# Kernel tuning notes

Measured on AMD Instinct MI355X. Metric: run time of the kernel, lower is better.

The kernel has to match this reference:

```python
import jax, jax.numpy as jnp
import numpy as np

N_NODES = 50000
N_EDGES = 800000
D_IN = 256
D_HID = 256
D_OUT = 128


def setup_inputs() -> dict:
    key = jax.random.key(0)
    ks = jax.random.split(key, 6)
    z = jax.random.normal(ks[0], (N_NODES, D_IN), dtype=jnp.float32)
    edge_index = jax.random.randint(ks[1], (2, N_EDGES), 0, N_NODES, dtype=jnp.int32)
    W1 = jax.random.normal(ks[2], (D_IN, D_HID), dtype=jnp.float32) / np.sqrt(D_IN).astype(np.float32)
    b1 = jnp.zeros((D_HID,), dtype=jnp.float32)
    W2 = jax.random.normal(ks[3], (D_HID, D_OUT), dtype=jnp.float32) / np.sqrt(D_HID).astype(np.float32)
    b2 = jnp.zeros((D_OUT,), dtype=jnp.float32)
    return {"z": z, "edge_index": edge_index, "W1": W1, "b1": b1, "W2": W2, "b2": b2}


def _gcn_conv(x, W, b, src, dst, n_nodes):
    """GCNConv: x' = D^{-1/2} (A + I) D^{-1/2} (x W) + b (symmetric norm, self-loops)."""
    x = x @ W  # [n, d_out] dense transform first (as in PyG GCNConv)
    loop = jnp.arange(n_nodes, dtype=src.dtype)
    s = jnp.concatenate([src, loop])  # add self-loops
    d = jnp.concatenate([dst, loop])
    deg = jax.ops.segment_sum(jnp.ones(s.shape, dtype=x.dtype), d, num_segments=n_nodes)
    dinv = jnp.where(deg > 0, jax.lax.rsqrt(deg), 0.0)
    norm = dinv[s] * dinv[d]  # per-edge symmetric normalization
    msgs = x[s] * norm[:, None]  # gather + scale
    out = jax.ops.segment_sum(msgs, d, num_segments=n_nodes)  # scatter-add
    return out + b


def reference(z, edge_index, W1, b1, W2, b2):
    src, dst = edge_index[0], edge_index[1]
    n = z.shape[0]
    h = jax.nn.relu(_gcn_conv(z, W1, b1, src, dst, n))
    return _gcn_conv(h, W2, b2, src, dst, n)
```

## Files before the change

### kernel.cpp

```cpp
#include <hip/hip_runtime.h>


#define N_NODES 50000
#define N_EDGES 800000
#define D_IN    256
#define D_HID   256
#define D_OUT   128

typedef unsigned int uint32;
typedef unsigned short u16;

typedef __attribute__((ext_vector_type(8))) short bf16x8;
typedef __attribute__((ext_vector_type(4))) float f32x4;

__device__ __forceinline__ u16 f2bf_rne(float f) {
    union { float f; uint32 u; } c; c.f = f;
    uint32 u = c.u;
    u += 0x7FFFu + ((u >> 16) & 1u);
    return (u16)(u >> 16);
}
__device__ __forceinline__ float bf_lo(uint32 p) {
    union { uint32 u; float f; } c; c.u = p << 16; return c.f;
}
__device__ __forceinline__ float bf_hi(uint32 p) {
    union { uint32 u; float f; } c; c.u = p & 0xFFFF0000u; return c.f;
}


__global__ __launch_bounds__(256) void prep_kernel(const float* __restrict__ z,
                                                   const int* __restrict__ dst,
                                                   const float* __restrict__ W1,
                                                   const float* __restrict__ W2,
                                                   u16* __restrict__ zb,
                                                   u16* __restrict__ w1t,
                                                   u16* __restrict__ w2t,
                                                   int* __restrict__ cnt) {
    const int g = blockIdx.x * 256 + threadIdx.x;
    const int GT = gridDim.x * 256;

    for (int c = g; c < N_NODES * D_IN / 8; c += GT) {
        int i = c * 8;
        float4 a = *(const float4*)(z + i);
        float4 d = *(const float4*)(z + i + 4);
        uint4 pk;
        pk.x = (uint32)f2bf_rne(a.x) | ((uint32)f2bf_rne(a.y) << 16);
        pk.y = (uint32)f2bf_rne(a.z) | ((uint32)f2bf_rne(a.w) << 16);
        pk.z = (uint32)f2bf_rne(d.x) | ((uint32)f2bf_rne(d.y) << 16);
        pk.w = (uint32)f2bf_rne(d.z) | ((uint32)f2bf_rne(d.w) << 16);
        *(uint4*)(zb + i) = pk;
    }
    for (int idx = g; idx < D_IN * D_HID + D_HID * D_OUT; idx += GT) {
        if (idx < D_IN * D_HID) {
            int nrow = idx >> 8, kcol = idx & 255;
            w1t[idx] = f2bf_rne(W1[kcol * D_HID + nrow]);
        } else {
            int j = idx - D_IN * D_HID;
            int nrow = j >> 8, kcol = j & 255;
            w2t[j] = f2bf_rne(W2[kcol * D_OUT + nrow]);
        }
    }
    for (int i = g; i < N_EDGES; i += GT) atomicAdd(&cnt[dst[i]], 1);
}


__global__ __launch_bounds__(256) void block_sum_kernel(const int* __restrict__ cnt,
                                                        float* __restrict__ dinv,
                                                        int* __restrict__ bsum, int n) {
    int b = blockIdx.x, t = threadIdx.x;
    int i = b * 256 + t;
    int v = 0;
    if (i < n) {
        v = cnt[i];
        dinv[i] = rsqrtf((float)(v + 1));
    }
    int r = v;
    #pragma unroll
    for (int off = 32; off >= 1; off >>= 1) r += __shfl_down(r, off, 64);
    __shared__ int ws[4];
    if ((t & 63) == 0) ws[t >> 6] = r;
    __syncthreads();
    if (t == 0) bsum[b] = ws[0] + ws[1] + ws[2] + ws[3];
}

__global__ __launch_bounds__(256) void scan_partials_kernel(const int* __restrict__ bsum,
                                                            int* __restrict__ boff,
                                                            int* __restrict__ row_ptr,
                                                            int nb, int n) {
    int t = threadIdx.x;
    int v = (t < nb) ? bsum[t] : 0;
    int lane = t & 63, w = t >> 6;
    int x = v;
    #pragma unroll
    for (int off = 1; off < 64; off <<= 1) {
        int u = __shfl_up(x, off, 64);
        if (lane >= off) x += u;
    }
    __shared__ int ws[4];
    if (lane == 63) ws[w] = x;
    __syncthreads();
    int base = 0;
    for (int i = 0; i < w; ++i) base += ws[i];
    int incl = base + x;
    if (t < nb) boff[t] = incl - v;
    if (t == 255) row_ptr[n] = incl;
}

__global__ __launch_bounds__(256) void scan_write_kernel(const int* __restrict__ cnt,
                                                         const int* __restrict__ boff,
                                                         int* __restrict__ row_ptr,
                                                         int* __restrict__ cursor, int n) {
    int b = blockIdx.x, t = threadIdx.x;
    int i = b * 256 + t;
    int v = (i < n) ? cnt[i] : 0;
    int lane = t & 63, w = t >> 6;
    int x = v;
    #pragma unroll
    for (int off = 1; off < 64; off <<= 1) {
        int u = __shfl_up(x, off, 64);
        if (lane >= off) x += u;
    }
    __shared__ int ws[4];
    if (lane == 63) ws[w] = x;
    __syncthreads();
    int base = boff[b];
    for (int i2 = 0; i2 < w; ++i2) base += ws[i2];
    int excl = base + (x - v);
    if (i < n) { row_ptr[i] = excl; cursor[i] = excl; }
}

__global__ void fill_kernel(const int* __restrict__ src, const int* __restrict__ dst,
                            int* __restrict__ cursor, int* __restrict__ col, int n_edges) {
    int i = blockIdx.x * blockDim.x + threadIdx.x;
    if (i < n_edges) {
        int d = dst[i];
        int s = src[i];
        int pos = atomicAdd(&cursor[d], 1);
        col[pos] = s;
    }
}


template <int NT>
__global__ __launch_bounds__(256, 4) void gemm_bf16_kernel(const u16* __restrict__ A,
                                                           const u16* __restrict__ BT,
                                                           u16* __restrict__ C, int M) {
    const int K = 256;
    __shared__ short As[128 * 32];
    __shared__ short Bs[128 * 32];

    const int m0 = blockIdx.x * 128;
    const int n0 = blockIdx.y * 128;
    const int t  = threadIdx.x;
    const int w  = t >> 6;
    const int lane = t & 63;
    const int lm = lane & 15;
    const int lq = lane >> 4;
    const int wm = w & 1;
    const int wn = w >> 1;

    f32x4 acc[4][4] = {};

    for (int k0 = 0; k0 < K; k0 += 32) {
        #pragma unroll
        for (int j = 0; j < 2; ++j) {
            int c = w * 128 + j * 64 + lane;
            int row = c >> 2;
            int kc = k0 + (c & 3) * 8;
            int gm = m0 + row; if (gm >= M) gm = M - 1;
            const u16* gpa = A  + (size_t)gm * K + kc;
            const u16* gpb = BT + (size_t)(n0 + row) * K + kc;
            __builtin_amdgcn_global_load_lds(
                (const __attribute__((address_space(1))) void*)gpa,
                (__attribute__((address_space(3))) void*)(As + (w * 128 + j * 64) * 8),
                16, 0, 0);
            __builtin_amdgcn_global_load_lds(
                (const __attribute__((address_space(1))) void*)gpb,
                (__attribute__((address_space(3))) void*)(Bs + (w * 128 + j * 64) * 8),
                16, 0, 0);
        }
        __syncthreads();

        bf16x8 af[4], bf[4];
        #pragma unroll
        for (int mt = 0; mt < 4; ++mt)
            af[mt] = *(const bf16x8*)&As[(wm * 64 + mt * 16 + lm) * 32 + lq * 8];
        #pragma unroll
        for (int nt = 0; nt < 4; ++nt)
            bf[nt] = *(const bf16x8*)&Bs[(wn * 64 + nt * 16 + lm) * 32 + lq * 8];

        #pragma unroll
        for (int mt = 0; mt < 4; ++mt)
            #pragma unroll
            for (int nt = 0; nt < 4; ++nt)
                acc[mt][nt] = __builtin_amdgcn_mfma_f32_16x16x32_bf16(
                    af[mt], bf[nt], acc[mt][nt], 0, 0, 0);

        __syncthreads();
    }

    #pragma unroll
    for (int mt = 0; mt < 4; ++mt) {
        #pragma unroll
        for (int r = 0; r < 4; ++r) {
            int gm = m0 + wm * 64 + mt * 16 + lq * 4 + r;
            if (gm < M) {
                #pragma unroll
                for (int nt = 0; nt < 4; ++nt) {
                    int gn = n0 + wn * 64 + nt * 16 + lm;
                    C[(size_t)gm * NT + gn] = f2bf_rne(acc[mt][nt][r]);
                }
            }
        }
    }
}


template <int D, int NSPLIT, bool RELU, bool OUTBF>
__global__ __launch_bounds__(256) void aggregate_kernel(const u16* __restrict__ x,
                                                        const int* __restrict__ row_ptr,
                                                        const int* __restrict__ col,
                                                        const float* __restrict__ dinv,
                                                        const float* __restrict__ bias,
                                                        void* __restrict__ outp, int n_nodes) {
    constexpr int DP  = D / NSPLIT;
    constexpr int VPL = DP / 64;
    const int b = blockIdx.x;
    const int part = b % NSPLIT;
    const int node = (b / NSPLIT) * 4 + (threadIdx.x >> 6);
    const int lane = threadIdx.x & 63;
    if (node >= n_nodes) return;
    const int c0 = part * DP + lane * VPL;

    float di = dinv[node];
    float acc[4][VPL] = {};

    {
        float w = di * di;
        const u16* xs = x + (size_t)node * D + c0;
        if constexpr (VPL == 4) {
            uint2 p = *(const uint2*)xs;
            acc[0][0] = bf_lo(p.x) * w;
            acc[0][1] = bf_hi(p.x) * w;
            acc[0][2] = bf_lo(p.y) * w;
            acc[0][3] = bf_hi(p.y) * w;
        } else {
            uint32 p = *(const uint32*)xs;
            acc[0][0] = bf_lo(p) * w;
            acc[0][1] = bf_hi(p) * w;
        }
    }

    int e0 = row_ptr[node], e1 = row_ptr[node + 1];
    int e = e0;
    for (; e + 4 <= e1; e += 4) {
        #pragma unroll
        for (int u = 0; u < 4; ++u) {
            int s  = col[e + u];
            float w = dinv[s] * di;
            const u16* xs = x + (size_t)s * D + c0;
            if constexpr (VPL == 4) {
                uint2 p = *(const uint2*)xs;
                acc[u][0] = fmaf(bf_lo(p.x), w, acc[u][0]);
                acc[u][1] = fmaf(bf_hi(p.x), w, acc[u][1]);
                acc[u][2] = fmaf(bf_lo(p.y), w, acc[u][2]);
                acc[u][3] = fmaf(bf_hi(p.y), w, acc[u][3]);
            } else {
                uint32 p = *(const uint32*)xs;
                acc[u][0] = fmaf(bf_lo(p), w, acc[u][0]);
                acc[u][1] = fmaf(bf_hi(p), w, acc[u][1]);
            }
        }
    }
    for (; e < e1; ++e) {
        int s  = col[e];
        float w = dinv[s] * di;
        const u16* xs = x + (size_t)s * D + c0;
        if constexpr (VPL == 4) {
            uint2 p = *(const uint2*)xs;
            acc[0][0] = fmaf(bf_lo(p.x), w, acc[0][0]);
            acc[0][1] = fmaf(bf_hi(p.x), w, acc[0][1]);
            acc[0][2] = fmaf(bf_lo(p.y), w, acc[0][2]);
            acc[0][3] = fmaf(bf_hi(p.y), w, acc[0][3]);
        } else {
            uint32 p = *(const uint32*)xs;
            acc[0][0] = fmaf(bf_lo(p), w, acc[0][0]);
            acc[0][1] = fmaf(bf_hi(p), w, acc[0][1]);
        }
    }

    float v[VPL];
    #pragma unroll
    for (int j = 0; j < VPL; ++j) {
        float s = acc[0][j] + acc[1][j] + acc[2][j] + acc[3][j] + bias[c0 + j];
        v[j] = RELU ? fmaxf(s, 0.0f) : s;
    }

    if constexpr (OUTBF) {
        u16* op = (u16*)outp + (size_t)node * D + c0;
        if constexpr (VPL == 4) {
            uint2 pk;
            pk.x = (uint32)f2bf_rne(v[0]) | ((uint32)f2bf_rne(v[1]) << 16);
            pk.y = (uint32)f2bf_rne(v[2]) | ((uint32)f2bf_rne(v[3]) << 16);
            *(uint2*)op = pk;
        } else {
            *(uint32*)op = (uint32)f2bf_rne(v[0]) | ((uint32)f2bf_rne(v[1]) << 16);
        }
    } else {
        float* op = (float*)outp + (size_t)node * D + c0;
        #pragma unroll
        for (int j = 0; j < VPL; ++j) op[j] = v[j];
    }
}


extern "C" void kernel_launch(void* const* d_in, const int* in_sizes, int n_in,
                              void* d_out, int out_size, void* d_ws, size_t ws_size,
                              hipStream_t stream) {
    const float* z  = (const float*)d_in[0];
    const int*   ei = (const int*)d_in[1];
    const float* W1 = (const float*)d_in[2];
    const float* b1 = (const float*)d_in[3];
    const float* W2 = (const float*)d_in[4];
    const float* b2 = (const float*)d_in[5];
    float* out = (float*)d_out;

    const int Nn = N_NODES, E = N_EDGES;
    const int* srcp = ei;
    const int* dstp = ei + E;

    char* ws = (char*)d_ws;
    size_t off = 0;
    auto alloc = [&](size_t bytes) -> char* {
        char* p = ws + off;
        off += (bytes + 511) & ~(size_t)511;
        return p;
    };
    u16*   zb     = (u16*)  alloc((size_t)Nn * D_IN * 2);
    u16*   w1t    = (u16*)  alloc((size_t)D_IN * D_HID * 2);
    u16*   w2t    = (u16*)  alloc((size_t)D_HID * D_OUT * 2);
    u16*   x1b    = (u16*)  alloc((size_t)Nn * D_HID * 2);
    u16*   hb     = (u16*)  alloc((size_t)Nn * D_HID * 2);
    u16*   h2b    = (u16*)  alloc((size_t)Nn * D_OUT * 2);
    int*   cnt    = (int*)  alloc((size_t)Nn * 4);
    float* dinv   = (float*)alloc((size_t)Nn * 4);
    int*   row_ptr= (int*)  alloc((size_t)(Nn + 1) * 4);
    int*   cursor = (int*)  alloc((size_t)Nn * 4);
    int*   col    = (int*)  alloc((size_t)E * 4);
    int*   bsum   = (int*)  alloc(256 * 4);
    int*   boff   = (int*)  alloc(256 * 4);

    const int nb = (Nn + 255) / 256;

    hipMemsetAsync(cnt, 0, (size_t)Nn * 4, stream);
    prep_kernel<<<1024, 256, 0, stream>>>(z, dstp, W1, W2, zb, w1t, w2t, cnt);
    block_sum_kernel<<<nb, 256, 0, stream>>>(cnt, dinv, bsum, Nn);
    scan_partials_kernel<<<1, 256, 0, stream>>>(bsum, boff, row_ptr, nb, Nn);
    scan_write_kernel<<<nb, 256, 0, stream>>>(cnt, boff, row_ptr, cursor, Nn);
    fill_kernel<<<(E + 255) / 256, 256, 0, stream>>>(srcp, dstp, cursor, col, E);

    {
        dim3 grid((Nn + 127) / 128, D_HID / 128);
        gemm_bf16_kernel<D_HID><<<grid, 256, 0, stream>>>(zb, w1t, x1b, Nn);
    }
    {
        int blocks = 2 * ((Nn + 3) / 4);
        aggregate_kernel<D_HID, 2, true, true><<<blocks, 256, 0, stream>>>(x1b, row_ptr, col, dinv, b1, hb, Nn);
    }

    {
        dim3 grid((Nn + 127) / 128, D_OUT / 128);
        gemm_bf16_kernel<D_OUT><<<grid, 256, 0, stream>>>(hb, w2t, h2b, Nn);
    }
    {
        int blocks = (Nn + 3) / 4;
        aggregate_kernel<D_OUT, 1, false, false><<<blocks, 256, 0, stream>>>(h2b, row_ptr, col, dinv, b2, out, Nn);
    }
}
```

Before: 334.5 us.

## Merge scan into single-block kernel, fuse CSR fill with GEMM1, drop aggregate split

Replaces the three-kernel degree scan with one 1024-thread single-block scan. The CSR fill (atomic cursor scatter) now runs as extra blocks of the first GEMM launch, so the two independent jobs overlap and a launch is saved. The layer-1 aggregation no longer splits the feature dimension across two blocks: one wavefront now covers all 256 columns, with 4 values per lane. The single-block scan serialises 50k elements on one CU, and the aggregate change alters parallelism and register use.

```diff
diff --git a/kernel.cpp b/kernel.cpp
--- a/kernel.cpp
+++ b/kernel.cpp
@@ -6,6 +6,10 @@
 #define D_IN    256
 #define D_HID   256
 #define D_OUT   128
+
+#define GEMM1_MT ((N_NODES + 127) / 128)
+#define GEMM1_BLOCKS (GEMM1_MT * (D_HID / 128))
+#define FILL_BLOCKS ((N_EDGES + 255) / 256)
 
 typedef unsigned int uint32;
 typedef unsigned short u16;
@@ -63,94 +67,76 @@
 }
 
 
-__global__ __launch_bounds__(256) void block_sum_kernel(const int* __restrict__ cnt,
-                                                        float* __restrict__ dinv,
-                                                        int* __restrict__ bsum, int n) {
-    int b = blockIdx.x, t = threadIdx.x;
-    int i = b * 256 + t;
-    int v = 0;
-    if (i < n) {
-        v = cnt[i];
-        dinv[i] = rsqrtf((float)(v + 1));
-    }
-    int r = v;
-    #pragma unroll
-    for (int off = 32; off >= 1; off >>= 1) r += __shfl_down(r, off, 64);
-    __shared__ int ws[4];
-    if ((t & 63) == 0) ws[t >> 6] = r;
+__global__ __launch_bounds__(1024) void scan_kernel(const int* __restrict__ cnt,
+                                                    float* __restrict__ dinv,
+                                                    int* __restrict__ row_ptr,
+                                                    int* __restrict__ cursor, int n) {
+    __shared__ int wtot[16];
+    __shared__ int carry;
+    const int t = threadIdx.x;
+    const int lane = t & 63, w = t >> 6;
+    if (t == 0) carry = 0;
     __syncthreads();
-    if (t == 0) bsum[b] = ws[0] + ws[1] + ws[2] + ws[3];
-}
-
-__global__ __launch_bounds__(256) void scan_partials_kernel(const int* __restrict__ bsum,
-                                                            int* __restrict__ boff,
-                                                            int* __restrict__ row_ptr,
-                                                            int nb, int n) {
-    int t = threadIdx.x;
-    int v = (t < nb) ? bsum[t] : 0;
-    int lane = t & 63, w = t >> 6;
-    int x = v;
-    #pragma unroll
-    for (int off = 1; off < 64; off <<= 1) {
-        int u = __shfl_up(x, off, 64);
-        if (lane >= off) x += u;
-    }
-    __shared__ int ws[4];
-    if (lane == 63) ws[w] = x;
-    __syncthreads();
-    int base = 0;
-    for (int i = 0; i < w; ++i) base += ws[i];
-    int incl = base + x;
-    if (t < nb) boff[t] = incl - v;
-    if (t == 255) row_ptr[n] = incl;
-}
-
-__global__ __launch_bounds__(256) void scan_write_kernel(const int* __restrict__ cnt,
-                                                         const int* __restrict__ boff,
-                                                         int* __restrict__ row_ptr,
-                                                         int* __restrict__ cursor, int n) {
-    int b = blockIdx.x, t = threadIdx.x;
-    int i = b * 256 + t;
-    int v = (i < n) ? cnt[i] : 0;
-    int lane = t & 63, w = t >> 6;
-    int x = v;
-    #pragma unroll
-    for (int off = 1; off < 64; off <<= 1) {
-        int u = __shfl_up(x, off, 64);
-        if (lane >= off) x += u;
-    }
-    __shared__ int ws[4];
-    if (lane == 63) ws[w] = x;
-    __syncthreads();
-    int base = boff[b];
-    for (int i2 = 0; i2 < w; ++i2) base += ws[i2];
-    int excl = base + (x - v);
-    if (i < n) { row_ptr[i] = excl; cursor[i] = excl; }
-}
-
-__global__ void fill_kernel(const int* __restrict__ src, const int* __restrict__ dst,
-                            int* __restrict__ cursor, int* __restrict__ col, int n_edges) {
-    int i = blockIdx.x * blockDim.x + threadIdx.x;
-    if (i < n_edges) {
-        int d = dst[i];
-        int s = src[i];
-        int pos = atomicAdd(&cursor[d], 1);
-        col[pos] = s;
-    }
-}
-
-
-template <int NT>
-__global__ __launch_bounds__(256, 4) void gemm_bf16_kernel(const u16* __restrict__ A,
-                                                           const u16* __restrict__ BT,
-                                                           u16* __restrict__ C, int M) {
-    const int K = 256;
+
+    for (int base = 0; base < n; base += 1024) {
+        int i = base + t;
+        int v = 0;
+        if (i < n) {
+            v = cnt[i];
+            dinv[i] = rsqrtf((float)(v + 1));
+        }
+        int x = v;
+        #pragma unroll
+        for (int off = 1; off < 64; off <<= 1) {
+            int u = __shfl_up(x, off, 64);
+            if (lane >= off) x += u;
+        }
+        if (lane == 63) wtot[w] = x;
+        __syncthreads();
+
+        int wbase = 0;
+        #pragma unroll
+        for (int j = 0; j < 16; ++j) if (j < w) wbase += wtot[j];
+        int excl = carry + wbase + x - v;
+        if (i < n) { row_ptr[i] = excl; cursor[i] = excl; }
+        __syncthreads();
+
+        if (t == 0) {
+            int s = 0;
+            #pragma unroll
+            for (int j = 0; j < 16; ++j) s += wtot[j];
+            carry += s;
+        }
+        __syncthreads();
+    }
+    if (t == 0) row_ptr[n] = carry;
+}
+
+
+__global__ __launch_bounds__(256, 4) void gemm1_fill_kernel(
+        const u16* __restrict__ A, const u16* __restrict__ BT,
+        u16* __restrict__ C,
+        const int* __restrict__ src, const int* __restrict__ dst,
+        int* __restrict__ cursor, int* __restrict__ col) {
     __shared__ short As[128 * 32];
     __shared__ short Bs[128 * 32];
-
-    const int m0 = blockIdx.x * 128;
-    const int n0 = blockIdx.y * 128;
-    const int t  = threadIdx.x;
+    const int b = blockIdx.x;
+    const int t = threadIdx.x;
+
+    if (b >= GEMM1_BLOCKS) {
+        int i = (b - GEMM1_BLOCKS) * 256 + t;
+        if (i < N_EDGES) {
+            int d = dst[i];
+            int s = src[i];
+            int pos = atomicAdd(&cursor[d], 1);
+            col[pos] = s;
+        }
+        return;
+    }
+
+    const int K = 256, M = N_NODES, NT = D_HID;
+    const int m0 = (b % GEMM1_MT) * 128;
+    const int n0 = (b / GEMM1_MT) * 128;
     const int w  = t >> 6;
     const int lane = t & 63;
     const int lm = lane & 15;
@@ -215,21 +201,93 @@
 }
 
 
-template <int D, int NSPLIT, bool RELU, bool OUTBF>
+template <int NT>
+__global__ __launch_bounds__(256, 4) void gemm_bf16_kernel(const u16* __restrict__ A,
+                                                           const u16* __restrict__ BT,
+                                                           u16* __restrict__ C, int M) {
+    const int K = 256;
+    __shared__ short As[128 * 32];
+    __shared__ short Bs[128 * 32];
+
+    const int m0 = blockIdx.x * 128;
+    const int n0 = blockIdx.y * 128;
+    const int t  = threadIdx.x;
+    const int w  = t >> 6;
+    const int lane = t & 63;
+    const int lm = lane & 15;
+    const int lq = lane >> 4;
+    const int wm = w & 1;
+    const int wn = w >> 1;
+
+    f32x4 acc[4][4] = {};
+
+    for (int k0 = 0; k0 < K; k0 += 32) {
+        #pragma unroll
+        for (int j = 0; j < 2; ++j) {
+            int c = w * 128 + j * 64 + lane;
+            int row = c >> 2;
+            int kc = k0 + (c & 3) * 8;
+            int gm = m0 + row; if (gm >= M) gm = M - 1;
+            const u16* gpa = A  + (size_t)gm * K + kc;
+            const u16* gpb = BT + (size_t)(n0 + row) * K + kc;
+            __builtin_amdgcn_global_load_lds(
+                (const __attribute__((address_space(1))) void*)gpa,
+                (__attribute__((address_space(3))) void*)(As + (w * 128 + j * 64) * 8),
+                16, 0, 0);
+            __builtin_amdgcn_global_load_lds(
+                (const __attribute__((address_space(1))) void*)gpb,
+                (__attribute__((address_space(3))) void*)(Bs + (w * 128 + j * 64) * 8),
+                16, 0, 0);
+        }
+        __syncthreads();
+
+        bf16x8 af[4], bf[4];
+        #pragma unroll
+        for (int mt = 0; mt < 4; ++mt)
+            af[mt] = *(const bf16x8*)&As[(wm * 64 + mt * 16 + lm) * 32 + lq * 8];
+        #pragma unroll
+        for (int nt = 0; nt < 4; ++nt)
+            bf[nt] = *(const bf16x8*)&Bs[(wn * 64 + nt * 16 + lm) * 32 + lq * 8];
+
+        #pragma unroll
+        for (int mt = 0; mt < 4; ++mt)
+            #pragma unroll
+            for (int nt = 0; nt < 4; ++nt)
+                acc[mt][nt] = __builtin_amdgcn_mfma_f32_16x16x32_bf16(
+                    af[mt], bf[nt], acc[mt][nt], 0, 0, 0);
+
+        __syncthreads();
+    }
+
+    #pragma unroll
+    for (int mt = 0; mt < 4; ++mt) {
+        #pragma unroll
+        for (int r = 0; r < 4; ++r) {
+            int gm = m0 + wm * 64 + mt * 16 + lq * 4 + r;
+            if (gm < M) {
+                #pragma unroll
+                for (int nt = 0; nt < 4; ++nt) {
+                    int gn = n0 + wn * 64 + nt * 16 + lm;
+                    C[(size_t)gm * NT + gn] = f2bf_rne(acc[mt][nt][r]);
+                }
+            }
+        }
+    }
+}
+
+
+template <int D, bool RELU, bool OUTBF>
 __global__ __launch_bounds__(256) void aggregate_kernel(const u16* __restrict__ x,
                                                         const int* __restrict__ row_ptr,
                                                         const int* __restrict__ col,
                                                         const float* __restrict__ dinv,
                                                         const float* __restrict__ bias,
                                                         void* __restrict__ outp, int n_nodes) {
-    constexpr int DP  = D / NSPLIT;
-    constexpr int VPL = DP / 64;
-    const int b = blockIdx.x;
-    const int part = b % NSPLIT;
-    const int node = (b / NSPLIT) * 4 + (threadIdx.x >> 6);
-    const int lane = threadIdx.x & 63;
+    constexpr int VPL = D / 64;
+    int node = (blockIdx.x * blockDim.x + threadIdx.x) >> 6;
+    int lane = threadIdx.x & 63;
     if (node >= n_nodes) return;
-    const int c0 = part * DP + lane * VPL;
+    const int c0 = lane * VPL;
 
     float di = dinv[node];
     float acc[4][VPL] = {};
@@ -346,33 +404,22 @@
     int*   row_ptr= (int*)  alloc((size_t)(Nn + 1) * 4);
     int*   cursor = (int*)  alloc((size_t)Nn * 4);
     int*   col    = (int*)  alloc((size_t)E * 4);
-    int*   bsum   = (int*)  alloc(256 * 4);
-    int*   boff   = (int*)  alloc(256 * 4);
-
-    const int nb = (Nn + 255) / 256;
 
     hipMemsetAsync(cnt, 0, (size_t)Nn * 4, stream);
     prep_kernel<<<1024, 256, 0, stream>>>(z, dstp, W1, W2, zb, w1t, w2t, cnt);
-    block_sum_kernel<<<nb, 256, 0, stream>>>(cnt, dinv, bsum, Nn);
-    scan_partials_kernel<<<1, 256, 0, stream>>>(bsum, boff, row_ptr, nb, Nn);
-    scan_write_kernel<<<nb, 256, 0, stream>>>(cnt, boff, row_ptr, cursor, Nn);
-    fill_kernel<<<(E + 255) / 256, 256, 0, stream>>>(srcp, dstp, cursor, col, E);
-
+    scan_kernel<<<1, 1024, 0, stream>>>(cnt, dinv, row_ptr, cursor, Nn);
+    gemm1_fill_kernel<<<GEMM1_BLOCKS + FILL_BLOCKS, 256, 0, stream>>>(
+        zb, w1t, x1b, srcp, dstp, cursor, col);
     {
-        dim3 grid((Nn + 127) / 128, D_HID / 128);
-        gemm_bf16_kernel<D_HID><<<grid, 256, 0, stream>>>(zb, w1t, x1b, Nn);
-    }
-    {
-        int blocks = 2 * ((Nn + 3) / 4);
-        aggregate_kernel<D_HID, 2, true, true><<<blocks, 256, 0, stream>>>(x1b, row_ptr, col, dinv, b1, hb, Nn);
-    }
-
+        int blocks = (Nn + 3) / 4;
+        aggregate_kernel<D_HID, true, true><<<blocks, 256, 0, stream>>>(x1b, row_ptr, col, dinv, b1, hb, Nn);
+    }
     {
         dim3 grid((Nn + 127) / 128, D_OUT / 128);
         gemm_bf16_kernel<D_OUT><<<grid, 256, 0, stream>>>(hb, w2t, h2b, Nn);
     }
     {
         int blocks = (Nn + 3) / 4;
-        aggregate_kernel<D_OUT, 1, false, false><<<blocks, 256, 0, stream>>>(h2b, row_ptr, col, dinv, b2, out, Nn);
-    }
-}
+        aggregate_kernel<D_OUT, false, false><<<blocks, 256, 0, stream>>>(h2b, row_ptr, col, dinv, b2, out, Nn);
+    }
+}
```

New measurement: 353.0 us. +5.5%, slower.

## Build CSR with atomic ranks and single-block scan; drop column split in aggregation

Applied to the files above, without the earlier changes.

The degree-count atomics now record each edge's rank within its destination row. That lets the fill kernel place edges at row_ptr+rank without a second atomic pass and without a cursor array. The three-kernel scan is replaced by one 1024-thread single-block scan that also computes dinv using int4/float4 accesses. The layer-1 aggregation no longer splits columns across two blocks, so each wavefront handles a full 256-wide row with 4 values per lane. The costs are an extra E-sized rank buffer, a serial single-block scan, and fewer, larger aggregation blocks.

```diff
diff --git a/kernel.cpp b/kernel.cpp
--- a/kernel.cpp
+++ b/kernel.cpp
@@ -34,7 +34,8 @@
                                                    u16* __restrict__ zb,
                                                    u16* __restrict__ w1t,
                                                    u16* __restrict__ w2t,
-                                                   int* __restrict__ cnt) {
+                                                   int* __restrict__ cnt,
+                                                   int* __restrict__ rank) {
     const int g = blockIdx.x * 256 + threadIdx.x;
     const int GT = gridDim.x * 256;
 
@@ -59,84 +60,73 @@
             w2t[j] = f2bf_rne(W2[kcol * D_OUT + nrow]);
         }
     }
-    for (int i = g; i < N_EDGES; i += GT) atomicAdd(&cnt[dst[i]], 1);
-}
-
-
-__global__ __launch_bounds__(256) void block_sum_kernel(const int* __restrict__ cnt,
-                                                        float* __restrict__ dinv,
-                                                        int* __restrict__ bsum, int n) {
-    int b = blockIdx.x, t = threadIdx.x;
-    int i = b * 256 + t;
-    int v = 0;
-    if (i < n) {
-        v = cnt[i];
-        dinv[i] = rsqrtf((float)(v + 1));
-    }
-    int r = v;
-    #pragma unroll
-    for (int off = 32; off >= 1; off >>= 1) r += __shfl_down(r, off, 64);
-    __shared__ int ws[4];
-    if ((t & 63) == 0) ws[t >> 6] = r;
+    for (int i = g; i < N_EDGES; i += GT)
+        rank[i] = atomicAdd(&cnt[dst[i]], 1);
+}
+
+
+__global__ __launch_bounds__(1024) void scan_kernel(const int* __restrict__ cnt,
+                                                    float* __restrict__ dinv,
+                                                    int* __restrict__ row_ptr, int n) {
+    __shared__ int wtot[16];
+    __shared__ int carry_s;
+    const int t = threadIdx.x;
+    const int lane = t & 63, w = t >> 6;
+    if (t == 0) carry_s = 0;
     __syncthreads();
-    if (t == 0) bsum[b] = ws[0] + ws[1] + ws[2] + ws[3];
-}
-
-__global__ __launch_bounds__(256) void scan_partials_kernel(const int* __restrict__ bsum,
-                                                            int* __restrict__ boff,
-                                                            int* __restrict__ row_ptr,
-                                                            int nb, int n) {
-    int t = threadIdx.x;
-    int v = (t < nb) ? bsum[t] : 0;
-    int lane = t & 63, w = t >> 6;
-    int x = v;
-    #pragma unroll
-    for (int off = 1; off < 64; off <<= 1) {
-        int u = __shfl_up(x, off, 64);
-        if (lane >= off) x += u;
-    }
-    __shared__ int ws[4];
-    if (lane == 63) ws[w] = x;
-    __syncthreads();
-    int base = 0;
-    for (int i = 0; i < w; ++i) base += ws[i];
-    int incl = base + x;
-    if (t < nb) boff[t] = incl - v;
-    if (t == 255) row_ptr[n] = incl;
-}
-
-__global__ __launch_bounds__(256) void scan_write_kernel(const int* __restrict__ cnt,
-                                                         const int* __restrict__ boff,
-                                                         int* __restrict__ row_ptr,
-                                                         int* __restrict__ cursor, int n) {
-    int b = blockIdx.x, t = threadIdx.x;
-    int i = b * 256 + t;
-    int v = (i < n) ? cnt[i] : 0;
-    int lane = t & 63, w = t >> 6;
-    int x = v;
-    #pragma unroll
-    for (int off = 1; off < 64; off <<= 1) {
-        int u = __shfl_up(x, off, 64);
-        if (lane >= off) x += u;
-    }
-    __shared__ int ws[4];
-    if (lane == 63) ws[w] = x;
-    __syncthreads();
-    int base = boff[b];
-    for (int i2 = 0; i2 < w; ++i2) base += ws[i2];
-    int excl = base + (x - v);
-    if (i < n) { row_ptr[i] = excl; cursor[i] = excl; }
-}
+
+    const int n4 = n >> 2;
+    for (int base = 0; base < n4; base += 1024) {
+        int i4 = base + t;
+        int4 v = make_int4(0, 0, 0, 0);
+        if (i4 < n4) v = ((const int4*)cnt)[i4];
+        int s = v.x + v.y + v.z + v.w;
+        int x = s;
+        #pragma unroll
+        for (int off = 1; off < 64; off <<= 1) {
+            int u = __shfl_up(x, off, 64);
+            if (lane >= off) x += u;
+        }
+        if (lane == 63) wtot[w] = x;
+        __syncthreads();
+
+        int wbase = 0;
+        #pragma unroll
+        for (int j = 0; j < 16; ++j) if (j < w) wbase += wtot[j];
+        int excl = carry_s + wbase + x - s;
+        if (i4 < n4) {
+            int4 rp;
+            rp.x = excl;
+            rp.y = rp.x + v.x;
+            rp.z = rp.y + v.y;
+            rp.w = rp.z + v.z;
+            ((int4*)row_ptr)[i4] = rp;
+            float4 dv;
+            dv.x = rsqrtf((float)(v.x + 1));
+            dv.y = rsqrtf((float)(v.y + 1));
+            dv.z = rsqrtf((float)(v.z + 1));
+            dv.w = rsqrtf((float)(v.w + 1));
+            ((float4*)dinv)[i4] = dv;
+        }
+        __syncthreads();
+        if (t == 0) {
+            int tot = 0;
+            #pragma unroll
+            for (int j = 0; j < 16; ++j) tot += wtot[j];
+            carry_s += tot;
+        }
+        __syncthreads();
+    }
+    if (t == 0) row_ptr[n] = carry_s;
+}
+
 
 __global__ void fill_kernel(const int* __restrict__ src, const int* __restrict__ dst,
-                            int* __restrict__ cursor, int* __restrict__ col, int n_edges) {
+                            const int* __restrict__ rank, const int* __restrict__ row_ptr,
+                            int* __restrict__ col, int n_edges) {
     int i = blockIdx.x * blockDim.x + threadIdx.x;
-    if (i < n_edges) {
-        int d = dst[i];
-        int s = src[i];
-        int pos = atomicAdd(&cursor[d], 1);
-        col[pos] = s;
-    }
+    if (i < n_edges)
+        col[row_ptr[dst[i]] + rank[i]] = src[i];
 }
 
 
@@ -215,21 +205,18 @@
 }
 
 
-template <int D, int NSPLIT, bool RELU, bool OUTBF>
+template <int D, bool RELU, bool OUTBF>
 __global__ __launch_bounds__(256) void aggregate_kernel(const u16* __restrict__ x,
                                                         const int* __restrict__ row_ptr,
                                                         const int* __restrict__ col,
                                                         const float* __restrict__ dinv,
                                                         const float* __restrict__ bias,
                                                         void* __restrict__ outp, int n_nodes) {
-    constexpr int DP  = D / NSPLIT;
-    constexpr int VPL = DP / 64;
-    const int b = blockIdx.x;
-    const int part = b % NSPLIT;
-    const int node = (b / NSPLIT) * 4 + (threadIdx.x >> 6);
-    const int lane = threadIdx.x & 63;
+    constexpr int VPL = D / 64;
+    int node = (blockIdx.x * blockDim.x + threadIdx.x) >> 6;
+    int lane = threadIdx.x & 63;
     if (node >= n_nodes) return;
-    const int c0 = part * DP + lane * VPL;
+    const int c0 = lane * VPL;
 
     float di = dinv[node];
     float acc[4][VPL] = {};
@@ -344,35 +331,27 @@
     int*   cnt    = (int*)  alloc((size_t)Nn * 4);
     float* dinv   = (float*)alloc((size_t)Nn * 4);
     int*   row_ptr= (int*)  alloc((size_t)(Nn + 1) * 4);
-    int*   cursor = (int*)  alloc((size_t)Nn * 4);
+    int*   rank   = (int*)  alloc((size_t)E * 4);
     int*   col    = (int*)  alloc((size_t)E * 4);
-    int*   bsum   = (int*)  alloc(256 * 4);
-    int*   boff   = (int*)  alloc(256 * 4);
-
-    const int nb = (Nn + 255) / 256;
 
     hipMemsetAsync(cnt, 0, (size_t)Nn * 4, stream);
-    prep_kernel<<<1024, 256, 0, stream>>>(z, dstp, W1, W2, zb, w1t, w2t, cnt);
-    block_sum_kernel<<<nb, 256, 0, stream>>>(cnt, dinv, bsum, Nn);
-    scan_partials_kernel<<<1, 256, 0, stream>>>(bsum, boff, row_ptr, nb, Nn);
-    scan_write_kernel<<<nb, 256, 0, stream>>>(cnt, boff, row_ptr, cursor, Nn);
-    fill_kernel<<<(E + 255) / 256, 256, 0, stream>>>(srcp, dstp, cursor, col, E);
-
+    prep_kernel<<<1024, 256, 0, stream>>>(z, dstp, W1, W2, zb, w1t, w2t, cnt, rank);
+    scan_kernel<<<1, 1024, 0, stream>>>(cnt, dinv, row_ptr, Nn);
+    fill_kernel<<<(E + 255) / 256, 256, 0, stream>>>(srcp, dstp, rank, row_ptr, col, E);
     {
         dim3 grid((Nn + 127) / 128, D_HID / 128);
         gemm_bf16_kernel<D_HID><<<grid, 256, 0, stream>>>(zb, w1t, x1b, Nn);
     }
     {
-        int blocks = 2 * ((Nn + 3) / 4);
-        aggregate_kernel<D_HID, 2, true, true><<<blocks, 256, 0, stream>>>(x1b, row_ptr, col, dinv, b1, hb, Nn);
-    }
-
+        int blocks = (Nn + 3) / 4;
+        aggregate_kernel<D_HID, true, true><<<blocks, 256, 0, stream>>>(x1b, row_ptr, col, dinv, b1, hb, Nn);
+    }
     {
         dim3 grid((Nn + 127) / 128, D_OUT / 128);
         gemm_bf16_kernel<D_OUT><<<grid, 256, 0, stream>>>(hb, w2t, h2b, Nn);
     }
     {
         int blocks = (Nn + 3) / 4;
-        aggregate_kernel<D_OUT, 1, false, false><<<blocks, 256, 0, stream>>>(h2b, row_ptr, col, dinv, b2, out, Nn);
-    }
-}
+        aggregate_kernel<D_OUT, false, false><<<blocks, 256, 0, stream>>>(h2b, row_ptr, col, dinv, b2, out, Nn);
+    }
+}
```

New measurement: 298.0 us. 1.12x faster.
